# Kernel optimization log

Hardware: AMD Instinct MI355X
Metric: run time of the kernel (lower is better)

## Reference

```python
import jax, jax.numpy as jnp
import numpy as np

EPS = 1e-5

def rotate_half(x):
    # interleaved pairs: (..., d*2) -> stack(-x2, x1) interleaved back
    x = x.reshape(*x.shape[:-1], -1, 2)
    x1, x2 = x[..., 0], x[..., 1]
    return jnp.stack((-x2, x1), axis=-1).reshape(*x.shape[:-2], -1)

def apply_rotary(freqs, x):
    # freqs: (b, n, d); x: (b, h, n, d) -> broadcast over heads (unsqueeze at dim=1)
    f = freqs[:, None, :, :]
    return x * jnp.cos(f) + rotate_half(x) * jnp.sin(f)

def layer_norm(x, g, b):
    mu = jnp.mean(x, axis=-1, keepdims=True)
    var = jnp.var(x, axis=-1, keepdims=True)
    return (x - mu) * jax.lax.rsqrt(var + EPS) * g + b

def setup_inputs() -> dict:
    key = jax.random.key(0)
    ks = jax.random.split(key, 10)
    b, nq, nkv, dim, h, dh = 8, 1024, 2048, 512, 8, 64
    inner = h * dh
    return {
        "x_query": jax.random.normal(ks[0], (b, nq, dim), jnp.float32),
        "x_context": jax.random.normal(ks[1], (b, nkv, dim), jnp.float32),
        "rotary_time_emb_query": jax.random.normal(ks[2], (b, nq, dh), jnp.float32),
        "rotary_time_emb_context": jax.random.normal(ks[3], (b, nkv, dh), jnp.float32),
        "context_mask": jnp.ones((b, nkv), dtype=bool),
        "ln_q_g": jnp.ones((dim,), jnp.float32),
        "ln_q_b": jnp.zeros((dim,), jnp.float32),
        "ln_c_g": jnp.ones((dim,), jnp.float32),
        "ln_c_b": jnp.zeros((dim,), jnp.float32),
        "Wq": jax.random.normal(ks[4], (dim, inner), jnp.float32) * 0.02,
        "Wkv": jax.random.normal(ks[5], (dim, 2 * inner), jnp.float32) * 0.02,
        "Wo": jax.random.normal(ks[6], (inner, dim), jnp.float32) * 0.02,
        "bo": jnp.zeros((dim,), jnp.float32),
    }

def reference(x_query, x_context, rotary_time_emb_query, rotary_time_emb_context,
              context_mask, ln_q_g, ln_q_b, ln_c_g, ln_c_b, Wq, Wkv, Wo, bo):
    h = 8
    xq = layer_norm(x_query, ln_q_g, ln_q_b)
    xc = layer_norm(x_context, ln_c_g, ln_c_b)
    q = xq @ Wq                       # (b, nq, inner)
    kv = xc @ Wkv                     # (b, nkv, 2*inner)
    k, v = jnp.split(kv, 2, axis=-1)
    split_heads = lambda t: t.reshape(t.shape[0], t.shape[1], h, -1).transpose(0, 2, 1, 3)
    q, k, v = split_heads(q), split_heads(k), split_heads(v)  # (b, h, n, dh)
    q = apply_rotary(rotary_time_emb_query, q)
    k = apply_rotary(rotary_time_emb_context, k)
    v = apply_rotary(rotary_time_emb_context, v)   # rotate_value=True
    dh = q.shape[-1]
    scale = 1.0 / jnp.sqrt(jnp.float32(dh))
    scores = jnp.einsum('bhqd,bhkd->bhqk', q, k) * scale
    neg = jnp.finfo(scores.dtype).min
    scores = jnp.where(context_mask[:, None, None, :], scores, neg)
    attn = jax.nn.softmax(scores, axis=-1)
    out = jnp.einsum('bhqk,bhkd->bhqd', attn, v)
    out = apply_rotary(-rotary_time_emb_query, out)  # inverse rotation
    out = out.transpose(0, 2, 1, 3).reshape(out.shape[0], out.shape[2], -1)  # (b, nq, inner)
    return out @ Wo + bo
```

## Files before the change

### kernel.cpp

```cpp
#include <hip/hip_runtime.h>
#include <hip/hip_bf16.h>
#include <math.h>

#define BB 8
#define NQ 1024
#define NKV 2048
#define DIM 512
#define H 8
#define DH 64
#define INNER 512
#define SCALE_LOG2E 0.18033688011112042f

typedef __bf16 bf16x8 __attribute__((ext_vector_type(8)));
typedef float f32x4 __attribute__((ext_vector_type(4)));
typedef unsigned int u32x4 __attribute__((ext_vector_type(4)));

__device__ __forceinline__ unsigned short f2bf(float f) {
  union { float f; unsigned int u; } v; v.f = f;
  unsigned int r = v.u + 0x7fffu + ((v.u >> 16) & 1u);
  return (unsigned short)(r >> 16);
}
__device__ __forceinline__ float bf2f(unsigned short h) {
  union { unsigned int u; float f; } v; v.u = ((unsigned int)h) << 16;
  return v.f;
}

__device__ __forceinline__ void gl_lds16(const unsigned short* g, unsigned short* l) {
  __builtin_amdgcn_global_load_lds(
      (const __attribute__((address_space(1))) unsigned int*)g,
      (__attribute__((address_space(3))) unsigned int*)l, 16, 0, 0);
}

__global__ __launch_bounds__(256) void prep_ln(
    const float* __restrict__ Wq, const float* __restrict__ Wkv,
    const float* __restrict__ Wo,
    unsigned short* __restrict__ WqT, unsigned short* __restrict__ WkvT,
    unsigned short* __restrict__ WohT, unsigned short* __restrict__ WolT,
    const float* __restrict__ xq, const float* __restrict__ xc,
    const float* __restrict__ gq, const float* __restrict__ bq,
    const float* __restrict__ gc, const float* __restrict__ bc,
    unsigned short* __restrict__ xq_bf, unsigned short* __restrict__ xc_bf) {
  __shared__ float T[64][65];
  __shared__ float red[8];
  int blk = blockIdx.x;
  int t = threadIdx.x;
  if (blk < 2048) {
    int wid = t >> 6, lane = t & 63;
    for (int rr = 0; rr < 12; ++rr) {
      int row = blk * 12 + rr;
      const float* x; const float* g; const float* bbv; unsigned short* outp;
      if (row < BB * NQ) {
        x = xq + (size_t)row * DIM; g = gq; bbv = bq; outp = xq_bf + (size_t)row * DIM;
      } else {
        int r2 = row - BB * NQ;
        x = xc + (size_t)r2 * DIM; g = gc; bbv = bc; outp = xc_bf + (size_t)r2 * DIM;
      }
      float2 v = *reinterpret_cast<const float2*>(x + t * 2);
      float s = v.x + v.y;
      float ss = v.x * v.x + v.y * v.y;
#pragma unroll
      for (int d = 1; d < 64; d <<= 1) { s += __shfl_xor(s, d); ss += __shfl_xor(ss, d); }
      if (lane == 0) { red[wid] = s; red[4 + wid] = ss; }
      __syncthreads();
      s = red[0] + red[1] + red[2] + red[3];
      ss = red[4] + red[5] + red[6] + red[7];
      __syncthreads();
      float mu = s * (1.0f / DIM);
      float var = ss * (1.0f / DIM) - mu * mu;
      float rs = rsqrtf(var + 1e-5f);
      float y0 = (v.x - mu) * rs * g[t * 2] + bbv[t * 2];
      float y1 = (v.y - mu) * rs * g[t * 2 + 1] + bbv[t * 2 + 1];
      ushort2 o; o.x = f2bf(y0); o.y = f2bf(y1);
      *reinterpret_cast<ushort2*>(outp + t * 2) = o;
    }
  } else {
    int blk2 = blk - 2048;
    const float* src; int Wd, ti, tj, mode;
    unsigned short* dst = nullptr;
    if (blk2 < 64) { src = Wq;  dst = WqT;  Wd = 512;  ti = blk2 >> 3; tj = blk2 & 7; mode = 0; }
    else if (blk2 < 192) { int b2 = blk2 - 64; src = Wkv; dst = WkvT; Wd = 1024; ti = b2 >> 4; tj = b2 & 15; mode = 0; }
    else { int b2 = blk2 - 192; src = Wo; Wd = 512; ti = b2 >> 3; tj = b2 & 7; mode = 1; }
#pragma unroll
    for (int i = 0; i < 16; ++i) {
      int idx = i * 256 + t;
      int r = idx >> 6, c = idx & 63;
      T[r][c] = src[(size_t)(ti * 64 + r) * Wd + tj * 64 + c];
    }
    __syncthreads();
#pragma unroll
    for (int i = 0; i < 16; ++i) {
      int idx = i * 256 + t;
      int n = idx >> 6, k = idx & 63;
      float v = T[k][n];
      size_t off = (size_t)(tj * 64 + n) * 512 + ti * 64 + k;
      if (mode == 0) {
        dst[off] = f2bf(v);
      } else {
        unsigned short hb = f2bf(v);
        WohT[off] = hb;
        WolT[off] = f2bf(v - bf2f(hb));
      }
    }
  }
}

__device__ __forceinline__ void gemm128_mainloop(
    const unsigned short* __restrict__ A, const unsigned short* __restrict__ WT,
    unsigned short* As, unsigned short* Ws,
    int rowBase, int colBase, f32x4 acc[4][4]) {
  const int t = threadIdx.x;
  const int w = t >> 6, l = t & 63;
  const int l15 = l & 15, lg = l >> 4, c7 = l15 & 7;
  const int wr = w >> 1, wc = w & 1;
  const int lrow = l >> 3;
  const int lchunk = (l & 7) ^ lrow;
  const int frag = (lg ^ c7) * 8;
  const unsigned short* Ag = A + (size_t)rowBase * 512;
  const unsigned short* Wg = WT + (size_t)colBase * 512;
#pragma unroll
  for (int m = 0; m < 4; ++m)
#pragma unroll
    for (int n = 0; n < 4; ++n) acc[m][n] = f32x4{0.f, 0.f, 0.f, 0.f};
  for (int kb = 0; kb < 512; kb += 64) {
#pragma unroll
    for (int i = 0; i < 4; ++i) {
      const int seg = w * 4 + i;
      const size_t goff = (size_t)(seg * 8 + lrow) * 512 + kb + lchunk * 8;
      gl_lds16(Ag + goff, As + seg * 512);
      gl_lds16(Wg + goff, Ws + seg * 512);
    }
    __syncthreads();
#pragma unroll
    for (int ks = 0; ks < 2; ++ks) {
      const int xo = ks ? 32 : 0;
      bf16x8 af[4], bf_[4];
#pragma unroll
      for (int m = 0; m < 4; ++m)
        af[m] = *reinterpret_cast<const bf16x8*>(
            &As[(wr * 64 + m * 16 + l15) * 64 + (frag ^ xo)]);
#pragma unroll
      for (int n = 0; n < 4; ++n)
        bf_[n] = *reinterpret_cast<const bf16x8*>(
            &Ws[(wc * 64 + n * 16 + l15) * 64 + (frag ^ xo)]);
#pragma unroll
      for (int m = 0; m < 4; ++m)
#pragma unroll
        for (int n = 0; n < 4; ++n)
          acc[m][n] = __builtin_amdgcn_mfma_f32_16x16x32_bf16(af[m], bf_[n], acc[m][n], 0, 0, 0);
    }
    __syncthreads();
  }
}

__global__ __launch_bounds__(256) void proj_fused(
    const unsigned short* __restrict__ xq_bf, const unsigned short* __restrict__ xc_bf,
    const unsigned short* __restrict__ WqT, const unsigned short* __restrict__ WkvT,
    const float* __restrict__ rotq, const float* __restrict__ rotc,
    const int* __restrict__ cmask,
    unsigned short* __restrict__ Qb, unsigned short* __restrict__ Kb,
    unsigned short* __restrict__ VTb) {
  __shared__ __align__(16) char smem[128 * 66 * 4];
  unsigned short* As = (unsigned short*)smem;
  unsigned short* Ws = (unsigned short*)(smem + 16384);
  float (*Cs)[66] = (float(*)[66])smem;
  const int t = threadIdx.x;
  const int w = t >> 6, l = t & 63;
  const int l15 = l & 15, lg = l >> 4;
  const int wr = w >> 1, wc = w & 1;
  f32x4 acc[4][4];
  int o = blockIdx.x;
  if (o < 1024) {
    int swz = ((o & 7) << 7) | (o >> 3);
    int bn = swz & 7, bm = swz >> 3;
    gemm128_mainloop(xc_bf, WkvT, As, Ws, bm * 128, bn * 128, acc);
#pragma unroll
    for (int hc = 0; hc < 2; ++hc) {
      if (wc == hc) {
#pragma unroll
        for (int m = 0; m < 4; ++m)
#pragma unroll
          for (int n = 0; n < 4; ++n)
#pragma unroll
            for (int r = 0; r < 4; ++r)
              Cs[wr * 64 + m * 16 + lg * 4 + r][n * 16 + l15] = acc[m][n][r];
      }
      __syncthreads();
      const int g = bn * 2 + hc;
      const int h = g & 7;
      if (g < 8) {
#pragma unroll
        for (int i = 0; i < 16; ++i) {
          int p = i * 256 + t;
          int row = p >> 5, pc = p & 31, d0 = pc * 2;
          int grow = bm * 128 + row;
          float c0 = Cs[row][d0], c1 = Cs[row][d0 + 1];
          const float* f = rotc + (size_t)grow * DH + d0;
          float f0 = f[0], f1 = f[1], s0, s1, co0, co1;
          __sincosf(f0, &s0, &co0);
          __sincosf(f1, &s1, &co1);
          float mf = cmask[grow] ? 1.f : 0.f;
          float o0 = (c0 * co0 - c1 * s0) * mf;
          float o1 = (c1 * co1 + c0 * s1) * mf;
          int b = grow >> 11, kk = grow & 2047;
          ushort2 ov; ov.x = f2bf(o0); ov.y = f2bf(o1);
          *reinterpret_cast<ushort2*>(Kb + (((size_t)(b * H + h) * NKV + kk) * DH + d0)) = ov;
        }
      } else {
#pragma unroll
        for (int i = 0; i < 16; ++i) {
          int p = i * 256 + t;
          int row = p >> 5, pc = p & 31, d0 = pc * 2;
          int grow = bm * 128 + row;
          float c0 = Cs[row][d0], c1 = Cs[row][d0 + 1];
          const float* f = rotc + (size_t)grow * DH + d0;
          float f0 = f[0], f1 = f[1], s0, s1, co0, co1;
          __sincosf(f0, &s0, &co0);
          __sincosf(f1, &s1, &co1);
          float mf = cmask[grow] ? 1.f : 0.f;
          Cs[row][d0]     = (c0 * co0 - c1 * s0) * mf;
          Cs[row][d0 + 1] = (c1 * co1 + c0 * s1) * mf;
        }
        __syncthreads();
        int oc = t & 7;
        int dd0 = t >> 3;
#pragma unroll
        for (int ch = 0; ch < 2; ++ch) {
          int ch64 = bm * 2 + ch;
          int bb = ch64 >> 5, chunk = ch64 & 31;
          unsigned short* vbase = VTb + (((size_t)(bb * H + h) * 32 + chunk) * 64) * 64;
#pragma unroll
          for (int half = 0; half < 2; ++half) {
            int d = dd0 + half * 32;
            u32x4 pack;
#pragma unroll
            for (int j2 = 0; j2 < 4; ++j2) {
              unsigned int lohi[2];
#pragma unroll
              for (int e = 0; e < 2; ++e) {
                int p = oc * 8 + j2 * 2 + e;
                int pp = p & 31;
                int kv = (p >> 5) * 32 + ((pp & 1) ? ((pp >> 1) + 16) : (pp >> 1));
                lohi[e] = f2bf(Cs[ch * 64 + kv][d]);
              }
              pack[j2] = lohi[0] | (lohi[1] << 16);
            }
            *reinterpret_cast<u32x4*>(vbase + d * 64 + oc * 8) = pack;
          }
        }
      }
      __syncthreads();
    }
  } else {
    int o2 = o - 1024;
    int swz = ((o2 & 7) << 5) | (o2 >> 3);
    int bn = swz & 3, bm = swz >> 2;
    gemm128_mainloop(xq_bf, WqT, As, Ws, bm * 128, bn * 128, acc);
#pragma unroll
    for (int hc = 0; hc < 2; ++hc) {
      if (wc == hc) {
#pragma unroll
        for (int m = 0; m < 4; ++m)
#pragma unroll
          for (int n = 0; n < 4; ++n)
#pragma unroll
            for (int r = 0; r < 4; ++r)
              Cs[wr * 64 + m * 16 + lg * 4 + r][n * 16 + l15] = acc[m][n][r];
      }
      __syncthreads();
      const int head = bn * 2 + hc;
#pragma unroll
      for (int i = 0; i < 16; ++i) {
        int p = i * 256 + t;
        int row = p >> 5, pc = p & 31, d0 = pc * 2;
        int grow = bm * 128 + row;
        float c0 = Cs[row][d0], c1 = Cs[row][d0 + 1];
        const float* f = rotq + (size_t)grow * DH + d0;
        float f0 = f[0], f1 = f[1], s0, s1, co0, co1;
        __sincosf(f0, &s0, &co0);
        __sincosf(f1, &s1, &co1);
        float o0 = (c0 * co0 - c1 * s0) * SCALE_LOG2E;
        float o1 = (c1 * co1 + c0 * s1) * SCALE_LOG2E;
        ushort2 ov; ov.x = f2bf(o0); ov.y = f2bf(o1);
        int b = grow >> 10, qq = grow & 1023;
        *reinterpret_cast<ushort2*>(Qb + (((size_t)(b * H + head) * NQ + qq) * DH + d0)) = ov;
      }
      __syncthreads();
    }
  }
}

__global__ __launch_bounds__(256) void attn_kernel(
    const unsigned short* __restrict__ Qb, const unsigned short* __restrict__ Kb,
    const unsigned short* __restrict__ VTb, const int* __restrict__ mask,
    const float* __restrict__ rotq,
    unsigned short* __restrict__ Ahb, unsigned short* __restrict__ Alb) {
  __shared__ unsigned short Ks[2 * 64 * 64];
  __shared__ unsigned short Vs[2 * 64 * 64];
  int ob = blockIdx.x;
  int swz = ((ob & 7) << 7) + (ob >> 3);
  int qb = swz & 15;
  int bh = swz >> 4;
  int b = bh >> 3, hh = bh & 7;
  int t = threadIdx.x, w = t >> 6, l = t & 63;
  int l15 = l & 15, lg = l >> 4;
  int c7 = l15 & 7;

  float nmasked;
  {
    const int* mrow = mask + b * NKV;
    float msum = 0.f;
#pragma unroll
    for (int i = 0; i < 8; ++i) {
      int4 m = *reinterpret_cast<const int4*>(mrow + l * 4 + i * 256);
      msum += (m.x ? 1.f : 0.f) + (m.y ? 1.f : 0.f) +
              (m.z ? 1.f : 0.f) + (m.w ? 1.f : 0.f);
    }
#pragma unroll
    for (int d = 1; d < 64; d <<= 1) msum += __shfl_xor(msum, d);
    nmasked = (float)NKV - msum;
  }

  const unsigned short* qrow = Qb + ((size_t)bh * NQ + qb * 64 + w * 16 + l15) * DH;
  bf16x8 qa0 = *reinterpret_cast<const bf16x8*>(qrow + lg * 8);
  bf16x8 qa1 = *reinterpret_cast<const bf16x8*>(qrow + 32 + lg * 8);

  float plsum = 0.f;
  f32x4 acc[4];
#pragma unroll
  for (int ct = 0; ct < 4; ++ct) acc[ct] = f32x4{0.f, 0.f, 0.f, 0.f};

  const int srow = t >> 2;
  const int sseg = (t & 3) * 16;
  const int sdst0 = srow * 64 + ((2 * (t & 3)) ^ (srow & 7)) * 8;
  const int frag = (lg ^ c7) * 8;
  const int kbase = l15 * 64 + frag;

  const unsigned short* gk = Kb + ((size_t)bh * NKV + srow) * DH + sseg;
  const unsigned short* gv = VTb + (((size_t)bh * 32) * 64 + srow) * 64 + sseg;

  bf16x8 kr0 = *reinterpret_cast<const bf16x8*>(gk);
  bf16x8 kr1 = *reinterpret_cast<const bf16x8*>(gk + 8);
  bf16x8 vr0 = *reinterpret_cast<const bf16x8*>(gv);
  bf16x8 vr1 = *reinterpret_cast<const bf16x8*>(gv + 8);
  gk += 4096; gv += 4096;

#pragma unroll 2
  for (int ic = 0; ic < NKV / 64; ++ic) {
    const int bo_ = (ic & 1) << 12;
    *reinterpret_cast<bf16x8*>(&Ks[bo_ + sdst0])       = kr0;
    *reinterpret_cast<bf16x8*>(&Ks[bo_ + (sdst0 ^ 8)]) = kr1;
    *reinterpret_cast<bf16x8*>(&Vs[bo_ + sdst0])       = vr0;
    *reinterpret_cast<bf16x8*>(&Vs[bo_ + (sdst0 ^ 8)]) = vr1;
    __syncthreads();
    if (ic + 1 < NKV / 64) {
      kr0 = *reinterpret_cast<const bf16x8*>(gk);
      kr1 = *reinterpret_cast<const bf16x8*>(gk + 8);
      vr0 = *reinterpret_cast<const bf16x8*>(gv);
      vr1 = *reinterpret_cast<const bf16x8*>(gv + 8);
      gk += 4096; gv += 4096;
    }
    f32x4 s[4];
    __builtin_amdgcn_s_setprio(1);
#pragma unroll
    for (int tt = 0; tt < 4; ++tt) {
      f32x4 z = f32x4{0.f, 0.f, 0.f, 0.f};
      bf16x8 k0 = *reinterpret_cast<const bf16x8*>(&Ks[bo_ + tt * 1024 + kbase]);
      z = __builtin_amdgcn_mfma_f32_16x16x32_bf16(k0, qa0, z, 0, 0, 0);
      bf16x8 k1 = *reinterpret_cast<const bf16x8*>(&Ks[bo_ + tt * 1024 + (kbase ^ 32)]);
      z = __builtin_amdgcn_mfma_f32_16x16x32_bf16(k1, qa1, z, 0, 0, 0);
      s[tt] = z;
    }
    __builtin_amdgcn_s_setprio(0);
    float p[4][4];
#pragma unroll
    for (int tt = 0; tt < 4; ++tt)
#pragma unroll
      for (int r = 0; r < 4; ++r) {
        float e;
        asm("v_exp_f32 %0, %1" : "=v"(e) : "v"(s[tt][r]));
        p[tt][r] = e;
      }
    plsum += ((p[0][0] + p[0][1]) + (p[0][2] + p[0][3])) +
             ((p[1][0] + p[1][1]) + (p[1][2] + p[1][3])) +
             ((p[2][0] + p[2][1]) + (p[2][2] + p[2][3])) +
             ((p[3][0] + p[3][1]) + (p[3][2] + p[3][3]));
    __builtin_amdgcn_s_setprio(1);
#pragma unroll
    for (int ks = 0; ks < 2; ++ks) {
      union { u32x4 u; bf16x8 b; } pa;
#pragma unroll
      for (int i = 0; i < 4; ++i)
        asm("v_cvt_pk_bf16_f32 %0, %1, %2"
            : "=v"(pa.u[i]) : "v"(p[ks * 2][i]), "v"(p[ks * 2 + 1][i]));
#pragma unroll
      for (int ct = 0; ct < 4; ++ct) {
        bf16x8 vb = *reinterpret_cast<const bf16x8*>(
            &Vs[bo_ + ct * 1024 + (kbase ^ (ks ? 32 : 0))]);
        acc[ct] = __builtin_amdgcn_mfma_f32_16x16x32_bf16(pa.b, vb, acc[ct], 0, 0, 0);
      }
    }
    __builtin_amdgcn_s_setprio(0);
  }
  plsum += __shfl_xor(plsum, 16);
  plsum += __shfl_xor(plsum, 32);
  float inv[4];
#pragma unroll
  for (int r = 0; r < 4; ++r)
    inv[r] = 1.0f / (__shfl(plsum, lg * 4 + r) - nmasked);

  int q0 = qb * 64 + w * 16 + lg * 4;
#pragma unroll
  for (int r = 0; r < 4; ++r) {
    int grow = b * NQ + q0 + r;
    const float* frow = rotq + (size_t)grow * DH;
    size_t obase = (size_t)grow * INNER + hh * DH;
#pragma unroll
    for (int ct = 0; ct < 4; ++ct) {
      int d = ct * 16 + l15;
      float x = acc[ct][r] * inv[r];
      float nb = __shfl_xor(x, 1);
      float f = frow[d];
      float sn, cs;
      __sincosf(f, &sn, &cs);
      float ov = (d & 1) ? (x * cs - nb * sn) : (x * cs + nb * sn);
      unsigned short hb = f2bf(ov);
      Ahb[obase + d] = hb;
      Alb[obase + d] = f2bf(ov - bf2f(hb));
    }
  }
}

__global__ __launch_bounds__(256) void final_gemm(
    const unsigned short* __restrict__ Ah, const unsigned short* __restrict__ Al,
    const unsigned short* __restrict__ Wh, const unsigned short* __restrict__ Wl,
    const float* __restrict__ bo, float* __restrict__ out) {
  __shared__ __align__(16) char smem[49152];
  unsigned short* AhS = (unsigned short*)smem;
  unsigned short* AlS = (unsigned short*)(smem + 16384);
  unsigned short* WhS = (unsigned short*)(smem + 32768);
  unsigned short* WlS = (unsigned short*)(smem + 40960);
  int o = blockIdx.x;
  int swz = ((o & 7) << 6) | (o >> 3);
  int bn = swz & 7, bm = swz >> 3;
  const int t = threadIdx.x;
  const int w = t >> 6, l = t & 63;
  const int l15 = l & 15, lg = l >> 4, c7 = l15 & 7;
  const int wr = w >> 1, wc = w & 1;
  const int lrow = l >> 3;
  const int lchunk = (l & 7) ^ lrow;
  const int frag = (lg ^ c7) * 8;
  const unsigned short* Agh = Ah + (size_t)bm * 128 * 512;
  const unsigned short* Agl = Al + (size_t)bm * 128 * 512;
  const unsigned short* Wgh = Wh + (size_t)bn * 64 * 512;
  const unsigned short* Wgl = Wl + (size_t)bn * 64 * 512;
  f32x4 acc[4][2];
#pragma unroll
  for (int m = 0; m < 4; ++m)
#pragma unroll
    for (int n = 0; n < 2; ++n) acc[m][n] = f32x4{0.f, 0.f, 0.f, 0.f};
  for (int kb = 0; kb < 512; kb += 64) {
#pragma unroll
    for (int i = 0; i < 4; ++i) {
      const int seg = w * 4 + i;
      const size_t goff = (size_t)(seg * 8 + lrow) * 512 + kb + lchunk * 8;
      gl_lds16(Agh + goff, AhS + seg * 512);
      gl_lds16(Agl + goff, AlS + seg * 512);
    }
#pragma unroll
    for (int i = 0; i < 2; ++i) {
      const int seg = w * 2 + i;
      const size_t goff = (size_t)(seg * 8 + lrow) * 512 + kb + lchunk * 8;
      gl_lds16(Wgh + goff, WhS + seg * 512);
      gl_lds16(Wgl + goff, WlS + seg * 512);
    }
    __syncthreads();
#pragma unroll
    for (int ks = 0; ks < 2; ++ks) {
      const int xo = ks ? 32 : 0;
      bf16x8 ah[4], al[4], wh[2], wl[2];
#pragma unroll
      for (int m = 0; m < 4; ++m) {
        const int off = (wr * 64 + m * 16 + l15) * 64 + (frag ^ xo);
        ah[m] = *reinterpret_cast<const bf16x8*>(&AhS[off]);
        al[m] = *reinterpret_cast<const bf16x8*>(&AlS[off]);
      }
#pragma unroll
      for (int n = 0; n < 2; ++n) {
        const int off = (wc * 32 + n * 16 + l15) * 64 + (frag ^ xo);
        wh[n] = *reinterpret_cast<const bf16x8*>(&WhS[off]);
        wl[n] = *reinterpret_cast<const bf16x8*>(&WlS[off]);
      }
#pragma unroll
      for (int m = 0; m < 4; ++m)
#pragma unroll
        for (int n = 0; n < 2; ++n) {
          acc[m][n] = __builtin_amdgcn_mfma_f32_16x16x32_bf16(ah[m], wh[n], acc[m][n], 0, 0, 0);
          acc[m][n] = __builtin_amdgcn_mfma_f32_16x16x32_bf16(al[m], wh[n], acc[m][n], 0, 0, 0);
          acc[m][n] = __builtin_amdgcn_mfma_f32_16x16x32_bf16(ah[m], wl[n], acc[m][n], 0, 0, 0);
        }
    }
    __syncthreads();
  }
  const int row0 = bm * 128 + wr * 64;
  const int col0 = bn * 64 + wc * 32;
#pragma unroll
  for (int m = 0; m < 4; ++m)
#pragma unroll
    for (int n = 0; n < 2; ++n) {
      int col = col0 + n * 16 + l15;
      float bv = bo[col];
#pragma unroll
      for (int r = 0; r < 4; ++r)
        out[(size_t)(row0 + m * 16 + lg * 4 + r) * 512 + col] = acc[m][n][r] + bv;
    }
}

extern "C" void kernel_launch(void* const* d_in, const int* in_sizes, int n_in,
                              void* d_out, int out_size, void* d_ws, size_t ws_size,
                              hipStream_t stream) {
  const float* x_query   = (const float*)d_in[0];
  const float* x_context = (const float*)d_in[1];
  const float* rot_q     = (const float*)d_in[2];
  const float* rot_c     = (const float*)d_in[3];
  const int*   cmask     = (const int*)d_in[4];
  const float* ln_q_g    = (const float*)d_in[5];
  const float* ln_q_b    = (const float*)d_in[6];
  const float* ln_c_g    = (const float*)d_in[7];
  const float* ln_c_b    = (const float*)d_in[8];
  const float* Wq        = (const float*)d_in[9];
  const float* Wkv       = (const float*)d_in[10];
  const float* Wo        = (const float*)d_in[11];
  const float* bo        = (const float*)d_in[12];
  float* out = (float*)d_out;

  char* ws = (char*)d_ws;
  unsigned short* xq_bf = (unsigned short*)(ws + 0);
  unsigned short* xc_bf = (unsigned short*)(ws + 8388608);
  unsigned short* Ahb   = (unsigned short*)(ws + 0);
  unsigned short* Alb   = (unsigned short*)(ws + 8388608);
  unsigned short* WqT   = (unsigned short*)(ws + 25165824);
  unsigned short* WkvT  = (unsigned short*)(ws + 25690112);
  unsigned short* Qb    = (unsigned short*)(ws + 26738688);
  unsigned short* Kb    = (unsigned short*)(ws + 35127296);
  unsigned short* VTb   = (unsigned short*)(ws + 51904512);
  unsigned short* WohT  = (unsigned short*)(ws + 68681728);
  unsigned short* WolT  = (unsigned short*)(ws + 69206016);

  prep_ln<<<dim3(2304), dim3(256), 0, stream>>>(
      Wq, Wkv, Wo, WqT, WkvT, WohT, WolT,
      x_query, x_context, ln_q_g, ln_q_b, ln_c_g, ln_c_b, xq_bf, xc_bf);
  proj_fused<<<dim3(1280), dim3(256), 0, stream>>>(
      xq_bf, xc_bf, WqT, WkvT, rot_q, rot_c, cmask, Qb, Kb, VTb);
  attn_kernel<<<dim3(1024), dim3(256), 0, stream>>>(Qb, Kb, VTb, cmask, rot_q, Ahb, Alb);
  final_gemm<<<dim3(512), dim3(256), 0, stream>>>(Ahb, Alb, WohT, WolT, bo, out);
}
```

Measured before the change: 134.9 us.

## Precompute rotary sin/cos tables in prep kernel and interleave Q/KV projection blocks

Adds a pass to the prep kernel that computes cos/sin for every query and context rotary angle once and stores them as interleaved float pairs. The projection and attention epilogues then read these tables instead of calling sincos. This removes repeated transcendental work: context angles were evaluated once per head group and query angles twice. The cost is extra memory traffic (8 bytes per angle written and reread). Projection block ordering is also changed so that one Q-projection block follows every four KV blocks, mixing the two workloads across the grid.

```diff
diff --git a/kernel.cpp b/kernel.cpp
--- a/kernel.cpp
+++ b/kernel.cpp
@@ -39,7 +39,9 @@
     const float* __restrict__ xq, const float* __restrict__ xc,
     const float* __restrict__ gq, const float* __restrict__ bq,
     const float* __restrict__ gc, const float* __restrict__ bc,
-    unsigned short* __restrict__ xq_bf, unsigned short* __restrict__ xc_bf) {
+    unsigned short* __restrict__ xq_bf, unsigned short* __restrict__ xc_bf,
+    const float* __restrict__ rotq, const float* __restrict__ rotc,
+    float* __restrict__ RSCq, float* __restrict__ RSCc) {
   __shared__ float T[64][65];
   __shared__ float red[8];
   int blk = blockIdx.x;
@@ -73,7 +75,7 @@
       ushort2 o; o.x = f2bf(y0); o.y = f2bf(y1);
       *reinterpret_cast<ushort2*>(outp + t * 2) = o;
     }
-  } else {
+  } else if (blk < 2304) {
     int blk2 = blk - 2048;
     const float* src; int Wd, ti, tj, mode;
     unsigned short* dst = nullptr;
@@ -100,6 +102,20 @@
         WohT[off] = hb;
         WolT[off] = f2bf(v - bf2f(hb));
       }
+    }
+  } else {
+    int o2 = blk - 2304;
+#pragma unroll
+    for (int e = 0; e < 6; ++e) {
+      int idx = o2 * 1536 + e * 256 + t;
+      float f = (idx < 524288) ? rotq[idx] : rotc[idx - 524288];
+      float sn, cs;
+      __sincosf(f, &sn, &cs);
+      float2 v2; v2.x = cs; v2.y = sn;
+      if (idx < 524288)
+        *reinterpret_cast<float2*>(RSCq + (size_t)idx * 2) = v2;
+      else
+        *reinterpret_cast<float2*>(RSCc + (size_t)(idx - 524288) * 2) = v2;
     }
   }
 }
@@ -155,7 +171,7 @@
 __global__ __launch_bounds__(256) void proj_fused(
     const unsigned short* __restrict__ xq_bf, const unsigned short* __restrict__ xc_bf,
     const unsigned short* __restrict__ WqT, const unsigned short* __restrict__ WkvT,
-    const float* __restrict__ rotq, const float* __restrict__ rotc,
+    const float* __restrict__ RSCq, const float* __restrict__ RSCc,
     const int* __restrict__ cmask,
     unsigned short* __restrict__ Qb, unsigned short* __restrict__ Kb,
     unsigned short* __restrict__ VTb) {
@@ -169,8 +185,11 @@
   const int wr = w >> 1, wc = w & 1;
   f32x4 acc[4][4];
   int o = blockIdx.x;
-  if (o < 1024) {
-    int swz = ((o & 7) << 7) | (o >> 3);
+  int q5 = o / 5;
+  int r5 = o - q5 * 5;
+  if (r5 != 4) {
+    int kvidx = q5 * 4 + r5;
+    int swz = ((kvidx & 7) << 7) | (kvidx >> 3);
     int bn = swz & 7, bm = swz >> 3;
     gemm128_mainloop(xc_bf, WkvT, As, Ws, bm * 128, bn * 128, acc);
 #pragma unroll
@@ -194,13 +213,11 @@
           int row = p >> 5, pc = p & 31, d0 = pc * 2;
           int grow = bm * 128 + row;
           float c0 = Cs[row][d0], c1 = Cs[row][d0 + 1];
-          const float* f = rotc + (size_t)grow * DH + d0;
-          float f0 = f[0], f1 = f[1], s0, s1, co0, co1;
-          __sincosf(f0, &s0, &co0);
-          __sincosf(f1, &s1, &co1);
+          float4 sc = *reinterpret_cast<const float4*>(
+              RSCc + (size_t)(grow * DH + d0) * 2);
           float mf = cmask[grow] ? 1.f : 0.f;
-          float o0 = (c0 * co0 - c1 * s0) * mf;
-          float o1 = (c1 * co1 + c0 * s1) * mf;
+          float o0 = (c0 * sc.x - c1 * sc.y) * mf;
+          float o1 = (c1 * sc.z + c0 * sc.w) * mf;
           int b = grow >> 11, kk = grow & 2047;
           ushort2 ov; ov.x = f2bf(o0); ov.y = f2bf(o1);
           *reinterpret_cast<ushort2*>(Kb + (((size_t)(b * H + h) * NKV + kk) * DH + d0)) = ov;
@@ -212,13 +229,11 @@
           int row = p >> 5, pc = p & 31, d0 = pc * 2;
           int grow = bm * 128 + row;
           float c0 = Cs[row][d0], c1 = Cs[row][d0 + 1];
-          const float* f = rotc + (size_t)grow * DH + d0;
-          float f0 = f[0], f1 = f[1], s0, s1, co0, co1;
-          __sincosf(f0, &s0, &co0);
-          __sincosf(f1, &s1, &co1);
+          float4 sc = *reinterpret_cast<const float4*>(
+              RSCc + (size_t)(grow * DH + d0) * 2);
           float mf = cmask[grow] ? 1.f : 0.f;
-          Cs[row][d0]     = (c0 * co0 - c1 * s0) * mf;
-          Cs[row][d0 + 1] = (c1 * co1 + c0 * s1) * mf;
+          Cs[row][d0]     = (c0 * sc.x - c1 * sc.y) * mf;
+          Cs[row][d0 + 1] = (c1 * sc.z + c0 * sc.w) * mf;
         }
         __syncthreads();
         int oc = t & 7;
@@ -251,7 +266,7 @@
       __syncthreads();
     }
   } else {
-    int o2 = o - 1024;
+    int o2 = q5;
     int swz = ((o2 & 7) << 5) | (o2 >> 3);
     int bn = swz & 3, bm = swz >> 2;
     gemm128_mainloop(xq_bf, WqT, As, Ws, bm * 128, bn * 128, acc);
@@ -274,12 +289,10 @@
         int row = p >> 5, pc = p & 31, d0 = pc * 2;
         int grow = bm * 128 + row;
         float c0 = Cs[row][d0], c1 = Cs[row][d0 + 1];
-        const float* f = rotq + (size_t)grow * DH + d0;
-        float f0 = f[0], f1 = f[1], s0, s1, co0, co1;
-        __sincosf(f0, &s0, &co0);
-        __sincosf(f1, &s1, &co1);
-        float o0 = (c0 * co0 - c1 * s0) * SCALE_LOG2E;
-        float o1 = (c1 * co1 + c0 * s1) * SCALE_LOG2E;
+        float4 sc = *reinterpret_cast<const float4*>(
+            RSCq + (size_t)(grow * DH + d0) * 2);
+        float o0 = (c0 * sc.x - c1 * sc.y) * SCALE_LOG2E;
+        float o1 = (c1 * sc.z + c0 * sc.w) * SCALE_LOG2E;
         ushort2 ov; ov.x = f2bf(o0); ov.y = f2bf(o1);
         int b = grow >> 10, qq = grow & 1023;
         *reinterpret_cast<ushort2*>(Qb + (((size_t)(b * H + head) * NQ + qq) * DH + d0)) = ov;
@@ -292,7 +305,7 @@
 __global__ __launch_bounds__(256) void attn_kernel(
     const unsigned short* __restrict__ Qb, const unsigned short* __restrict__ Kb,
     const unsigned short* __restrict__ VTb, const int* __restrict__ mask,
-    const float* __restrict__ rotq,
+    const float* __restrict__ RSCq,
     unsigned short* __restrict__ Ahb, unsigned short* __restrict__ Alb) {
   __shared__ unsigned short Ks[2 * 64 * 64];
   __shared__ unsigned short Vs[2 * 64 * 64];
@@ -412,17 +425,15 @@
 #pragma unroll
   for (int r = 0; r < 4; ++r) {
     int grow = b * NQ + q0 + r;
-    const float* frow = rotq + (size_t)grow * DH;
+    const float* scrow = RSCq + (size_t)grow * DH * 2;
     size_t obase = (size_t)grow * INNER + hh * DH;
 #pragma unroll
     for (int ct = 0; ct < 4; ++ct) {
       int d = ct * 16 + l15;
       float x = acc[ct][r] * inv[r];
       float nb = __shfl_xor(x, 1);
-      float f = frow[d];
-      float sn, cs;
-      __sincosf(f, &sn, &cs);
-      float ov = (d & 1) ? (x * cs - nb * sn) : (x * cs + nb * sn);
+      float2 sc = *reinterpret_cast<const float2*>(scrow + d * 2);
+      float ov = (d & 1) ? (x * sc.x - nb * sc.y) : (x * sc.x + nb * sc.y);
       unsigned short hb = f2bf(ov);
       Ahb[obase + d] = hb;
       Alb[obase + d] = f2bf(ov - bf2f(hb));
@@ -545,12 +556,15 @@
   unsigned short* VTb   = (unsigned short*)(ws + 51904512);
   unsigned short* WohT  = (unsigned short*)(ws + 68681728);
   unsigned short* WolT  = (unsigned short*)(ws + 69206016);
-
-  prep_ln<<<dim3(2304), dim3(256), 0, stream>>>(
+  float*          RSCq  = (float*)(ws + 69730304);
+  float*          RSCc  = (float*)(ws + 73924608);
+
+  prep_ln<<<dim3(3328), dim3(256), 0, stream>>>(
       Wq, Wkv, Wo, WqT, WkvT, WohT, WolT,
-      x_query, x_context, ln_q_g, ln_q_b, ln_c_g, ln_c_b, xq_bf, xc_bf);
+      x_query, x_context, ln_q_g, ln_q_b, ln_c_g, ln_c_b, xq_bf, xc_bf,
+      rot_q, rot_c, RSCq, RSCc);
   proj_fused<<<dim3(1280), dim3(256), 0, stream>>>(
-      xq_bf, xc_bf, WqT, WkvT, rot_q, rot_c, cmask, Qb, Kb, VTb);
-  attn_kernel<<<dim3(1024), dim3(256), 0, stream>>>(Qb, Kb, VTb, cmask, rot_q, Ahb, Alb);
+      xq_bf, xc_bf, WqT, WkvT, RSCq, RSCc, cmask, Qb, Kb, VTb);
+  attn_kernel<<<dim3(1024), dim3(256), 0, stream>>>(Qb, Kb, VTb, cmask, RSCq, Ahb, Alb);
   final_gemm<<<dim3(512), dim3(256), 0, stream>>>(Ahb, Alb, WohT, WolT, bo, out);
 }
```

Result: slower. 141.7 us (+5.0%).

## Double-buffer LDS tiles in projection GEMM mainloop to overlap loads with MFMA

Applied to the files above, without the earlier changes.

Splits the shared-memory A/W tiles into two buffers and prefetches the next k-block via global-to-LDS loads while the current block is consumed by MFMAs. The aim is to hide global load latency in the QKV projection GEMM. LDS use grows from about 34KB to 64KB per block, which may reduce occupancy. The single __syncthreads per iteration must cover both the buffer swap and the prefetch completion.

```diff
diff --git a/kernel.cpp b/kernel.cpp
--- a/kernel.cpp
+++ b/kernel.cpp
@@ -106,8 +106,7 @@
 
 __device__ __forceinline__ void gemm128_mainloop(
     const unsigned short* __restrict__ A, const unsigned short* __restrict__ WT,
-    unsigned short* As, unsigned short* Ws,
-    int rowBase, int colBase, f32x4 acc[4][4]) {
+    char* smem, int rowBase, int colBase, f32x4 acc[4][4]) {
   const int t = threadIdx.x;
   const int w = t >> 6, l = t & 63;
   const int l15 = l & 15, lg = l >> 4, c7 = l15 & 7;
@@ -117,19 +116,33 @@
   const int frag = (lg ^ c7) * 8;
   const unsigned short* Ag = A + (size_t)rowBase * 512;
   const unsigned short* Wg = WT + (size_t)colBase * 512;
+  unsigned short* AsB[2] = { (unsigned short*)smem, (unsigned short*)(smem + 32768) };
+  unsigned short* WsB[2] = { (unsigned short*)(smem + 16384), (unsigned short*)(smem + 49152) };
 #pragma unroll
   for (int m = 0; m < 4; ++m)
 #pragma unroll
     for (int n = 0; n < 4; ++n) acc[m][n] = f32x4{0.f, 0.f, 0.f, 0.f};
-  for (int kb = 0; kb < 512; kb += 64) {
-#pragma unroll
-    for (int i = 0; i < 4; ++i) {
-      const int seg = w * 4 + i;
-      const size_t goff = (size_t)(seg * 8 + lrow) * 512 + kb + lchunk * 8;
-      gl_lds16(Ag + goff, As + seg * 512);
-      gl_lds16(Wg + goff, Ws + seg * 512);
-    }
-    __syncthreads();
+#pragma unroll
+  for (int i = 0; i < 4; ++i) {
+    const int seg = w * 4 + i;
+    const size_t goff = (size_t)(seg * 8 + lrow) * 512 + lchunk * 8;
+    gl_lds16(Ag + goff, AsB[0] + seg * 512);
+    gl_lds16(Wg + goff, WsB[0] + seg * 512);
+  }
+  __syncthreads();
+  for (int s = 0; s < 8; ++s) {
+    const int cur = s & 1;
+    if (s + 1 < 8) {
+#pragma unroll
+      for (int i = 0; i < 4; ++i) {
+        const int seg = w * 4 + i;
+        const size_t goff = (size_t)(seg * 8 + lrow) * 512 + (s + 1) * 64 + lchunk * 8;
+        gl_lds16(Ag + goff, AsB[cur ^ 1] + seg * 512);
+        gl_lds16(Wg + goff, WsB[cur ^ 1] + seg * 512);
+      }
+    }
+    const unsigned short* As = AsB[cur];
+    const unsigned short* Ws = WsB[cur];
 #pragma unroll
     for (int ks = 0; ks < 2; ++ks) {
       const int xo = ks ? 32 : 0;
@@ -159,9 +172,7 @@
     const int* __restrict__ cmask,
     unsigned short* __restrict__ Qb, unsigned short* __restrict__ Kb,
     unsigned short* __restrict__ VTb) {
-  __shared__ __align__(16) char smem[128 * 66 * 4];
-  unsigned short* As = (unsigned short*)smem;
-  unsigned short* Ws = (unsigned short*)(smem + 16384);
+  __shared__ __align__(16) char smem[65536];
   float (*Cs)[66] = (float(*)[66])smem;
   const int t = threadIdx.x;
   const int w = t >> 6, l = t & 63;
@@ -172,7 +183,7 @@
   if (o < 1024) {
     int swz = ((o & 7) << 7) | (o >> 3);
     int bn = swz & 7, bm = swz >> 3;
-    gemm128_mainloop(xc_bf, WkvT, As, Ws, bm * 128, bn * 128, acc);
+    gemm128_mainloop(xc_bf, WkvT, smem, bm * 128, bn * 128, acc);
 #pragma unroll
     for (int hc = 0; hc < 2; ++hc) {
       if (wc == hc) {
@@ -254,7 +265,7 @@
     int o2 = o - 1024;
     int swz = ((o2 & 7) << 5) | (o2 >> 3);
     int bn = swz & 3, bm = swz >> 2;
-    gemm128_mainloop(xq_bf, WqT, As, Ws, bm * 128, bn * 128, acc);
+    gemm128_mainloop(xq_bf, WqT, smem, bm * 128, bn * 128, acc);
 #pragma unroll
     for (int hc = 0; hc < 2; ++hc) {
       if (wc == hc) {
```

After: 155.0 us. +14.8%, slower.
